# Kernel tuning notes

Measured on AMD Instinct MI355X. Metric: run time of the kernel, lower is better.

The kernel has to match this reference:

```python
import jax, jax.numpy as jnp
import numpy as np

N, DIN, DOUT, E, K = 65536, 256, 256, 8, 2

def setup_inputs() -> dict:
    key = jax.random.key(0)
    k1, k2, k3, k4 = jax.random.split(key, 4)
    x = jax.random.normal(k1, (N, DIN), dtype=jnp.float32)
    Wr = jax.random.normal(k2, (DIN, E), dtype=jnp.float32) * (DIN ** -0.5)   # router Linear (no bias)
    We = jax.random.normal(k3, (E, DIN, DOUT), dtype=jnp.float32) * (DIN ** -0.5)  # expert Linear weights
    be = jax.random.normal(k4, (E, DOUT), dtype=jnp.float32) * 0.01               # expert Linear biases
    return {"x": x, "Wr": Wr, "We": We, "be": be}

def reference(x, Wr, We, be):
    # router: softmax over experts (eval mode -> no noise)
    probs = jax.nn.softmax(x @ Wr, axis=1)                    # [N, E]
    w, sel = jax.lax.top_k(probs, K)                          # [N, K]
    w = w / jnp.sum(w, axis=1, keepdims=True)                 # renormalize top-k weights
    # dense combine weights: scatter top-k weights back to [N, E]
    combine = jnp.zeros_like(probs).at[jnp.arange(x.shape[0])[:, None], sel].add(w)
    # all-expert outputs, then weighted combine (same math as gather/matmul/index_add loop)
    y_all = jnp.einsum('ni,eio->neo', x, We) + be[None, :, :]  # [N, E, DOUT]
    out = jnp.einsum('neo,ne->no', y_all, combine)             # [N, DOUT]
    return out
```

## Files before the change

kernel.cpp:

```cpp
#include <hip/hip_runtime.h>

#define N_TOK 65536
#define DIN   256
#define DOUT  256
#define NEXP  8
#define NPAIR 28

typedef __bf16 bf16x8 __attribute__((ext_vector_type(8)));
typedef __bf16 bf16x4 __attribute__((ext_vector_type(4)));
typedef float  f32x4  __attribute__((ext_vector_type(4)));

__device__ __forceinline__ void cp16_g2l(const void* g, void* l) {
  auto gp = (const __attribute__((address_space(1))) unsigned int*)(unsigned long long)g;
  auto lp = (__attribute__((address_space(3))) unsigned int*)(unsigned long long)l;
  __builtin_amdgcn_global_load_lds(gp, lp, 16, 0, 0);
}

__global__ __launch_bounds__(256) void prep_kernel(const float* __restrict__ We,
                                                   __bf16* __restrict__ Wt,
                                                   int* __restrict__ cnt) {
  __shared__ float T[64 * 65];
  int bid = blockIdx.x;
  if (bid == 0 && threadIdx.x < NPAIR) cnt[threadIdx.x] = 0;
  int e = bid >> 4;
  int tk = (bid >> 2) & 3, tn = bid & 3;
  int k0 = tk * 64, n0 = tn * 64;
  int tid = threadIdx.x;
  int cr = tid >> 6;
  int cc = tid & 63;
#pragma unroll
  for (int i = 0; i < 16; i++) {
    int k = i * 4 + cr;
    T[cc * 65 + k] = We[(size_t)(e * 256 + k0 + k) * 256 + n0 + cc];
  }
  __syncthreads();
#pragma unroll
  for (int i = 0; i < 16; i++) {
    int n = i * 4 + cr;
    Wt[(size_t)(e * 256 + n0 + n) * 256 + k0 + cc] = (__bf16)T[n * 65 + cc];
  }
}

__global__ __launch_bounds__(256) void router_kernel(const float* __restrict__ x,
                                                     const float* __restrict__ Wr,
                                                     __bf16* __restrict__ xb,
                                                     int* __restrict__ cnt,
                                                     unsigned short* __restrict__ pidx,
                                                     float* __restrict__ pw) {
  __shared__ float WrL[DIN * NEXP];
  __shared__ int lcnt[NPAIR];
  __shared__ int gbase[NPAIR];
  int tid = threadIdx.x;
  for (int j = tid; j < DIN * NEXP / 4; j += 256)
    *(float4*)&WrL[j * 4] = *(const float4*)&Wr[j * 4];
  if (tid < NPAIR) lcnt[tid] = 0;
  __syncthreads();

  int token = blockIdx.x * 256 + tid;
  const float4* xr = (const float4*)(x + (size_t)token * DIN);
  __bf16* xbr = xb + (size_t)token * DIN;

  float acc[NEXP];
#pragma unroll
  for (int e = 0; e < NEXP; e++) acc[e] = 0.f;

#pragma unroll 8
  for (int i4 = 0; i4 < DIN / 4; i4++) {
    float4 v = xr[i4];
    bf16x4 bv;
    bv[0] = (__bf16)v.x; bv[1] = (__bf16)v.y; bv[2] = (__bf16)v.z; bv[3] = (__bf16)v.w;
    *(bf16x4*)(xbr + i4 * 4) = bv;
    const float* w0 = &WrL[(i4 * 4) * NEXP];
#pragma unroll
    for (int e = 0; e < NEXP; e++)
      acc[e] += v.x * w0[e] + v.y * w0[NEXP + e] + v.z * w0[2 * NEXP + e] + v.w * w0[3 * NEXP + e];
  }

  int best = 0;
#pragma unroll
  for (int e = 1; e < NEXP; e++) if (acc[e] > acc[best]) best = e;
  int sec = (best == 0) ? 1 : 0;
#pragma unroll
  for (int e = 0; e < NEXP; e++)
    if (e != best && e != sec && acc[e] > acc[sec]) sec = e;
  float l3 = -1e30f;
#pragma unroll
  for (int e = 0; e < NEXP; e++)
    if (e != best && e != sec) l3 = fmaxf(l3, acc[e]);

  float diff = acc[sec] - acc[best];
  bool need = (acc[sec] - l3) < 5e-3f;
  if (__any(need)) {
    if (need) {
      double d[NEXP];
#pragma unroll
      for (int e = 0; e < NEXP; e++) d[e] = 0.0;
      for (int i4 = 0; i4 < DIN / 4; i4++) {
        float4 v = xr[i4];
        const float* w0 = &WrL[(i4 * 4) * NEXP];
#pragma unroll
        for (int e = 0; e < NEXP; e++)
          d[e] += (double)v.x * w0[e] + (double)v.y * w0[NEXP + e] +
                  (double)v.z * w0[2 * NEXP + e] + (double)v.w * w0[3 * NEXP + e];
      }
      best = 0;
#pragma unroll
      for (int e = 1; e < NEXP; e++) if (d[e] > d[best]) best = e;
      sec = (best == 0) ? 1 : 0;
#pragma unroll
      for (int e = 0; e < NEXP; e++)
        if (e != best && e != sec && d[e] > d[sec]) sec = e;
      diff = (float)(d[sec] - d[best]);
    }
  }

  float wb = 1.f / (1.f + expf(diff));
  int a, b2; float wa;
  if (best < sec) { a = best; b2 = sec; wa = wb; }
  else            { a = sec;  b2 = best; wa = 1.f - wb; }
  int p = a * (15 - a) / 2 + (b2 - a - 1);

  int lpos = atomicAdd(&lcnt[p], 1);
  __syncthreads();
  if (tid < NPAIR) gbase[tid] = atomicAdd(&cnt[tid], lcnt[tid]);
  __syncthreads();
  int pos = gbase[p] + lpos;
  pidx[p * N_TOK + pos] = (unsigned short)token;
  pw[p * N_TOK + pos] = wa;
}

__global__ __launch_bounds__(256) void moe_gemm_kernel(const __bf16* __restrict__ xb,
                                                       const __bf16* __restrict__ Wt,
                                                       const float* __restrict__ be,
                                                       const int* __restrict__ cnt,
                                                       const unsigned short* __restrict__ pidx,
                                                       const float* __restrict__ pw,
                                                       float* __restrict__ out) {
  __shared__ __bf16 As[128 * 64];
  __shared__ unsigned short tokL[128];
  __shared__ float wL[128];
  __shared__ int meta[4];

  int tid = threadIdx.x;
  int tile = blockIdx.x >> 2;
  int nh = blockIdx.x & 3;

  if (tid == 0) {
    int s = 0, pp = -1, lt = 0, c = 0;
    for (int q = 0; q < NPAIR; q++) {
      int cq = cnt[q];
      int tq = (cq + 127) >> 7;
      if (tile < s + tq) { pp = q; lt = tile - s; c = cq; break; }
      s += tq;
    }
    meta[0] = pp; meta[1] = lt; meta[2] = c;
  }
  __syncthreads();
  int p = meta[0];
  if (p < 0) return;
  int lt = meta[1], cnt_p = meta[2];

  int a = 0, rem = p;
  while (rem >= 7 - a) { rem -= 7 - a; a++; }
  int b2 = a + 1 + rem;
  int r0 = lt * 128;

  if (tid < 128) {
    int gr = r0 + tid;
    tokL[tid] = (gr < cnt_p) ? pidx[p * N_TOK + gr] : (unsigned short)0;
    wL[tid]   = (gr < cnt_p) ? pw[p * N_TOK + gr] : 0.f;
  }
  __syncthreads();

  const int lane = tid & 63, wid = tid >> 6;
  const int wm = wid & 1, wn = wid >> 1;
  const int c16 = lane & 15, quad = lane >> 4;

  const int r_base = tid >> 3;
  const int s8 = (tid & 7) ^ (r_base & 7);
  size_t grow[4];
#pragma unroll
  for (int i = 0; i < 4; i++)
    grow[i] = (size_t)tokL[r_base + 32 * i] * DIN + s8 * 8;

  const __bf16* WtA = Wt + ((size_t)a * DOUT + nh * 64) * DIN;
  const __bf16* WtB = Wt + ((size_t)b2 * DOUT + nh * 64) * DIN;

  f32x4 accA[4][2], accB[4][2];
#pragma unroll
  for (int mi = 0; mi < 4; mi++)
#pragma unroll
    for (int ni = 0; ni < 2; ni++)
#pragma unroll
      for (int r = 0; r < 4; r++) { accA[mi][ni][r] = 0.f; accB[mi][ni][r] = 0.f; }

  for (int kc = 0; kc < 4; kc++) {
#pragma unroll
    for (int i = 0; i < 4; i++) {
      int slot = tid + 256 * i;
      cp16_g2l(xb + grow[i] + kc * 64, &As[slot * 8]);
    }
    __builtin_amdgcn_s_waitcnt(0x0F70);
    __syncthreads();
#pragma unroll
    for (int ks = 0; ks < 2; ks++) {
      bf16x8 af[4], ba[2], bb[2];
#pragma unroll
      for (int mi = 0; mi < 4; mi++) {
        int row = wm * 64 + mi * 16 + c16;
        int oct = ks * 4 + quad;
        af[mi] = *(const bf16x8*)&As[(row * 8 + (oct ^ (row & 7))) * 8];
      }
#pragma unroll
      for (int ni = 0; ni < 2; ni++) {
        int col = wn * 32 + ni * 16 + c16;
        int koff = kc * 64 + ks * 32 + quad * 8;
        ba[ni] = *(const bf16x8*)&WtA[(size_t)col * DIN + koff];
        bb[ni] = *(const bf16x8*)&WtB[(size_t)col * DIN + koff];
      }
#pragma unroll
      for (int mi = 0; mi < 4; mi++)
#pragma unroll
        for (int ni = 0; ni < 2; ni++) {
          accA[mi][ni] = __builtin_amdgcn_mfma_f32_16x16x32_bf16(af[mi], ba[ni], accA[mi][ni], 0, 0, 0);
          accB[mi][ni] = __builtin_amdgcn_mfma_f32_16x16x32_bf16(af[mi], bb[ni], accB[mi][ni], 0, 0, 0);
        }
    }
    __syncthreads();
  }

#pragma unroll
  for (int ni = 0; ni < 2; ni++) {
    int gcol = nh * 64 + wn * 32 + ni * 16 + c16;
    float bea = be[a * DOUT + gcol];
    float beb = be[b2 * DOUT + gcol];
#pragma unroll
    for (int mi = 0; mi < 4; mi++) {
#pragma unroll
      for (int r = 0; r < 4; r++) {
        int row = wm * 64 + mi * 16 + quad * 4 + r;
        if (r0 + row < cnt_p) {
          float w = wL[row];
          out[(size_t)tokL[row] * DOUT + gcol] =
              w * (accA[mi][ni][r] + bea) + (1.f - w) * (accB[mi][ni][r] + beb);
        }
      }
    }
  }
}

extern "C" void kernel_launch(void* const* d_in, const int* in_sizes, int n_in,
                              void* d_out, int out_size, void* d_ws, size_t ws_size,
                              hipStream_t stream) {
  const float* x  = (const float*)d_in[0];
  const float* Wr = (const float*)d_in[1];
  const float* We = (const float*)d_in[2];
  const float* be = (const float*)d_in[3];
  float* out = (float*)d_out;

  char* w = (char*)d_ws;
  __bf16* Wt = (__bf16*)w;
  __bf16* xb = (__bf16*)(w + (1u << 20));
  int* cnt = (int*)(w + (33u << 20));
  unsigned short* pidx = (unsigned short*)(w + (33u << 20) + 512);
  float* pw = (float*)(w + (33u << 20) + 512 + (size_t)NPAIR * N_TOK * 2);

  prep_kernel<<<128, 256, 0, stream>>>(We, Wt, cnt);
  router_kernel<<<N_TOK / 256, 256, 0, stream>>>(x, Wr, xb, cnt, pidx, pw);
  moe_gemm_kernel<<<540 * 4, 256, 0, stream>>>(xb, Wt, be, cnt, pidx, pw, out);
}
```

Baseline: 224.9 us.

## Coalesce router x loads via swizzled LDS staging and read Wr uniformly

The router kernel now runs one 64-thread block per 64 tokens. It loads x in coalesced 32-column chunks, stages them through a XOR-swizzled shared-memory tile, and writes the bf16 copy coalesced. Before, each thread streamed its own row with strided accesses. Wr is now read directly from global memory with wave-uniform addresses (likely scalar loads) instead of being copied into LDS, and the next chunk is prefetched while the current one is computed. In exchange there are more blocks and two barriers per chunk.

```diff
diff --git a/kernel.cpp b/kernel.cpp
--- a/kernel.cpp
+++ b/kernel.cpp
@@ -41,39 +41,60 @@
   }
 }
 
-__global__ __launch_bounds__(256) void router_kernel(const float* __restrict__ x,
-                                                     const float* __restrict__ Wr,
-                                                     __bf16* __restrict__ xb,
-                                                     int* __restrict__ cnt,
-                                                     unsigned short* __restrict__ pidx,
-                                                     float* __restrict__ pw) {
-  __shared__ float WrL[DIN * NEXP];
+__global__ __launch_bounds__(64) void router_kernel(const float* __restrict__ x,
+                                                    const float* __restrict__ Wr,
+                                                    __bf16* __restrict__ xb,
+                                                    int* __restrict__ cnt,
+                                                    unsigned short* __restrict__ pidx,
+                                                    float* __restrict__ pw) {
+  __shared__ float X[64 * 32];
   __shared__ int lcnt[NPAIR];
   __shared__ int gbase[NPAIR];
   int tid = threadIdx.x;
-  for (int j = tid; j < DIN * NEXP / 4; j += 256)
-    *(float4*)&WrL[j * 4] = *(const float4*)&Wr[j * 4];
   if (tid < NPAIR) lcnt[tid] = 0;
-  __syncthreads();
-
-  int token = blockIdx.x * 256 + tid;
-  const float4* xr = (const float4*)(x + (size_t)token * DIN);
-  __bf16* xbr = xb + (size_t)token * DIN;
+
+  int tokBase = blockIdx.x * 64;
+  int token = tokBase + tid;
+
+  const int sr = tid >> 3;
+  const int so = tid & 7;
+  const int po = so ^ sr;
+  const int ro = tid & 7;
 
   float acc[NEXP];
 #pragma unroll
   for (int e = 0; e < NEXP; e++) acc[e] = 0.f;
 
-#pragma unroll 8
-  for (int i4 = 0; i4 < DIN / 4; i4++) {
-    float4 v = xr[i4];
-    bf16x4 bv;
-    bv[0] = (__bf16)v.x; bv[1] = (__bf16)v.y; bv[2] = (__bf16)v.z; bv[3] = (__bf16)v.w;
-    *(bf16x4*)(xbr + i4 * 4) = bv;
-    const float* w0 = &WrL[(i4 * 4) * NEXP];
-#pragma unroll
-    for (int e = 0; e < NEXP; e++)
-      acc[e] += v.x * w0[e] + v.y * w0[NEXP + e] + v.z * w0[2 * NEXP + e] + v.w * w0[3 * NEXP + e];
+  float4 v[8];
+#pragma unroll
+  for (int i = 0; i < 8; i++)
+    v[i] = *(const float4*)&x[(size_t)(tokBase + i * 8 + sr) * DIN + so * 4];
+
+  for (int kc = 0; kc < 8; kc++) {
+#pragma unroll
+    for (int i = 0; i < 8; i++) {
+      int r = i * 8 + sr;
+      *(float4*)&X[((r * 8 + po)) * 4] = v[i];
+      bf16x4 bv;
+      bv[0] = (__bf16)v[i].x; bv[1] = (__bf16)v[i].y;
+      bv[2] = (__bf16)v[i].z; bv[3] = (__bf16)v[i].w;
+      *(bf16x4*)&xb[(size_t)(tokBase + r) * DIN + kc * 32 + so * 4] = bv;
+    }
+    __syncthreads();
+    if (kc < 7) {
+#pragma unroll
+      for (int i = 0; i < 8; i++)
+        v[i] = *(const float4*)&x[(size_t)(tokBase + i * 8 + sr) * DIN + (kc + 1) * 32 + so * 4];
+    }
+#pragma unroll
+    for (int i4 = 0; i4 < 8; i4++) {
+      float4 xv = *(const float4*)&X[((tid * 8 + (i4 ^ ro))) * 4];
+      const float* w0 = &Wr[(kc * 32 + i4 * 4) * NEXP];
+#pragma unroll
+      for (int e = 0; e < NEXP; e++)
+        acc[e] += xv.x * w0[e] + xv.y * w0[NEXP + e] + xv.z * w0[2 * NEXP + e] + xv.w * w0[3 * NEXP + e];
+    }
+    __syncthreads();
   }
 
   int best = 0;
@@ -92,16 +113,17 @@
   bool need = (acc[sec] - l3) < 5e-3f;
   if (__any(need)) {
     if (need) {
+      const float4* xr = (const float4*)(x + (size_t)token * DIN);
       double d[NEXP];
 #pragma unroll
       for (int e = 0; e < NEXP; e++) d[e] = 0.0;
       for (int i4 = 0; i4 < DIN / 4; i4++) {
-        float4 v = xr[i4];
-        const float* w0 = &WrL[(i4 * 4) * NEXP];
+        float4 vv = xr[i4];
+        const float* w0 = &Wr[(i4 * 4) * NEXP];
 #pragma unroll
         for (int e = 0; e < NEXP; e++)
-          d[e] += (double)v.x * w0[e] + (double)v.y * w0[NEXP + e] +
-                  (double)v.z * w0[2 * NEXP + e] + (double)v.w * w0[3 * NEXP + e];
+          d[e] += (double)vv.x * w0[e] + (double)vv.y * w0[NEXP + e] +
+                  (double)vv.z * w0[2 * NEXP + e] + (double)vv.w * w0[3 * NEXP + e];
       }
       best = 0;
 #pragma unroll
@@ -266,6 +288,6 @@
   float* pw = (float*)(w + (33u << 20) + 512 + (size_t)NPAIR * N_TOK * 2);
 
   prep_kernel<<<128, 256, 0, stream>>>(We, Wt, cnt);
-  router_kernel<<<N_TOK / 256, 256, 0, stream>>>(x, Wr, xb, cnt, pidx, pw);
+  router_kernel<<<N_TOK / 64, 64, 0, stream>>>(x, Wr, xb, cnt, pidx, pw);
   moe_gemm_kernel<<<540 * 4, 256, 0, stream>>>(xb, Wt, be, cnt, pidx, pw, out);
 }
```

Result: slower. 235.4 us (+4.6%).
